# Kernel tuning notes

Measured on AMD Instinct MI355X. Metric: run time of the kernel, lower is better.

Reference implementation:

```python
import jax, jax.numpy as jnp
import numpy as np

B, S, D, H = 4, 2048, 1024, 16
HD = D // H


def setup_inputs() -> dict:
    key = jax.random.key(0)
    ks = jax.random.split(key, 12)
    sc = 1.0 / np.sqrt(D)
    inp = {
        'q': jax.random.normal(ks[0], (B, S, D), jnp.float32),
        'k': jax.random.normal(ks[1], (B, S, D), jnp.float32),
        'v': jax.random.normal(ks[2], (B, S, D), jnp.float32),
        # causal mask: 1 where masked (upper triangle), broadcasts over batch/heads
        'mask': jnp.triu(jnp.ones((S, S), jnp.float32), k=1),
        'Wq': jax.random.normal(ks[3], (D, D), jnp.float32) * sc,
        'bq': jax.random.normal(ks[4], (D,), jnp.float32) * sc,
        'Wk': jax.random.normal(ks[5], (D, D), jnp.float32) * sc,
        'bk': jax.random.normal(ks[6], (D,), jnp.float32) * sc,
        'Wv': jax.random.normal(ks[7], (D, D), jnp.float32) * sc,
        'bv': jax.random.normal(ks[8], (D,), jnp.float32) * sc,
        'Wo': jax.random.normal(ks[9], (D, D), jnp.float32) * sc,
        'bo': jax.random.normal(ks[10], (D,), jnp.float32) * sc,
    }
    return inp


def _split_heads(x):
    # [B,S,D] -> [B,H,S,HD]
    return x.reshape(B, S, H, HD).transpose(0, 2, 1, 3)


def reference(q, k, v, mask, Wq, bq, Wk, bk, Wv, bv, Wo, bo):
    qw = q @ Wq + bq
    kw = k @ Wk + bk
    vw = v @ Wv + bv
    qh, kh, vh = _split_heads(qw), _split_heads(kw), _split_heads(vw)
    scores = jnp.einsum('bhqd,bhkd->bhqk', qh, kh) / jnp.sqrt(jnp.float32(HD))
    scores = scores + mask * (-1e20)
    weights = jax.nn.softmax(scores, axis=-1)
    attn = jnp.einsum('bhqk,bhkd->bhqd', weights, vh)
    attn = attn.transpose(0, 2, 1, 3).reshape(B, S, D)
    return attn @ Wo + bo
```

## Files before the change

### kernel.cpp

```cpp
#include <hip/hip_runtime.h>
#include <hip/hip_bf16.h>
#include <stdint.h>

#define B_ 4
#define S_ 2048
#define D_ 1024
#define H_ 16
#define HD_ 64

typedef __bf16 bf16_t;
typedef __bf16 bf16x8 __attribute__((ext_vector_type(8)));
typedef __bf16 bf16x2_t __attribute__((ext_vector_type(2)));
typedef float f32x4 __attribute__((ext_vector_type(4)));
typedef int i32x4 __attribute__((ext_vector_type(4)));

#define MFMA(a, b, c) __builtin_amdgcn_mfma_f32_16x16x32_bf16((a), (b), (c), 0, 0, 0)
#define LOG2E 1.44269504088896340736f

__device__ __forceinline__ void gload_lds16(const void* g, void* l) {
  __builtin_amdgcn_global_load_lds(
      (const __attribute__((address_space(1))) uint32_t*)g,
      (__attribute__((address_space(3))) uint32_t*)l, 16, 0, 0);
}

__device__ __forceinline__ float max3f(float a, float b, float c) {
  float d;
  asm("v_max3_f32 %0, %1, %2, %3" : "=v"(d) : "v"(a), "v"(b), "v"(c));
  return d;
}

__global__ __launch_bounds__(256) void wt_kernel(const float* __restrict__ Wq,
                                                 const float* __restrict__ Wk,
                                                 const float* __restrict__ Wv,
                                                 const float* __restrict__ Wo,
                                                 bf16_t* __restrict__ wt0) {
  __shared__ float t[32][33];
  const int z = blockIdx.z;
  const float* w_ = z == 0 ? Wq : (z == 1 ? Wk : (z == 2 ? Wv : Wo));
  bf16_t* wt = wt0 + (size_t)z * (1u << 20);
  const int tx = threadIdx.x & 31, ty = threadIdx.x >> 5;
  const int n0 = blockIdx.x * 32, k0 = blockIdx.y * 32;
#pragma unroll
  for (int i = 0; i < 4; i++)
    t[ty + i * 8][tx] = w_[(size_t)(k0 + ty + i * 8) * D_ + n0 + tx];
  __syncthreads();
#pragma unroll
  for (int i = 0; i < 4; i++)
    wt[(size_t)(n0 + ty + i * 8) * D_ + k0 + tx] = (bf16_t)t[tx][ty + i * 8];
}

__global__ __launch_bounds__(256) void qkv_gemm(const float* __restrict__ qi,
                                                const float* __restrict__ ki,
                                                const float* __restrict__ vi,
                                                const bf16_t* __restrict__ wt0,
                                                const float* __restrict__ bq,
                                                const float* __restrict__ bk,
                                                const float* __restrict__ bv,
                                                bf16_t* __restrict__ out0) {
  constexpr int K = D_;
  __shared__ bf16_t smem[17408];
  bf16_t* alds = smem;
  bf16_t* blds = smem + 8192;

  const int z = blockIdx.z;
  const float* A = z == 0 ? qi : (z == 1 ? ki : vi);
  const bf16_t* WT = wt0 + (size_t)z * (1u << 20);
  const float* bias = z == 0 ? bq : (z == 1 ? bk : bv);
  bf16_t* out = out0 + (size_t)z * (8u << 20);

  const int tid = threadIdx.x;
  const int w = tid >> 6, l = tid & 63;
  const int lr = l & 15, lg = l >> 4;
  const int wm = w >> 1, wn = w & 1;
  const int ib = (int)blockIdx.y * (int)gridDim.x + (int)blockIdx.x;
  const int swz = (ib & 7) * 64 + (ib >> 3);
  const int m0 = (swz >> 3) * 128, n0 = (swz & 7) * 128;

  f32x4 acc[4][4];
#pragma unroll
  for (int mt = 0; mt < 4; mt++)
#pragma unroll
    for (int nt = 0; nt < 4; nt++) {
      f32x4 zz = {0.f, 0.f, 0.f, 0.f};
      acc[mt][nt] = zz;
    }

  for (int k0 = 0; k0 < K; k0 += 64) {
#pragma unroll
    for (int c = 0; c < 4; c++) {
      int ci = c * 256 + w * 64 + l;
      int row = ci >> 3, kc = ci & 7;
      int ks = kc ^ (row & 7);
      gload_lds16(WT + (size_t)(n0 + row) * K + k0 + ks * 8,
                  blds + (size_t)(c * 256 + w * 64) * 8);
    }
#pragma unroll
    for (int c = 0; c < 4; c++) {
      int ci = c * 256 + tid;
      int row = ci >> 3, kc = ci & 7;
      int ks = kc ^ (row & 7);
      const float* src = A + (size_t)(m0 + row) * K + k0 + ks * 8;
      float4 x0 = ((const float4*)src)[0];
      float4 x1 = ((const float4*)src)[1];
      bf16x8 vv;
      vv[0] = (bf16_t)x0.x; vv[1] = (bf16_t)x0.y; vv[2] = (bf16_t)x0.z; vv[3] = (bf16_t)x0.w;
      vv[4] = (bf16_t)x1.x; vv[5] = (bf16_t)x1.y; vv[6] = (bf16_t)x1.z; vv[7] = (bf16_t)x1.w;
      *reinterpret_cast<bf16x8*>(alds + (size_t)ci * 8) = vv;
    }
    __syncthreads();
#pragma unroll
    for (int kk = 0; kk < 2; kk++) {
      bf16x8 af[4], bfr[4];
#pragma unroll
      for (int mt = 0; mt < 4; mt++) {
        int row = wm * 64 + mt * 16 + lr;
        int kc = kk * 4 + lg;
        af[mt] = *reinterpret_cast<const bf16x8*>(alds + row * 64 + ((kc ^ (row & 7)) * 8));
      }
#pragma unroll
      for (int nt = 0; nt < 4; nt++) {
        int row = wn * 64 + nt * 16 + lr;
        int kc = kk * 4 + lg;
        bfr[nt] = *reinterpret_cast<const bf16x8*>(blds + row * 64 + ((kc ^ (row & 7)) * 8));
      }
#pragma unroll
      for (int mt = 0; mt < 4; mt++)
#pragma unroll
        for (int nt = 0; nt < 4; nt++)
          acc[mt][nt] = MFMA(af[mt], bfr[nt], acc[mt][nt]);
    }
    __syncthreads();
  }

  float bn[4];
#pragma unroll
  for (int nt = 0; nt < 4; nt++) bn[nt] = bias[n0 + wn * 64 + nt * 16 + lr];

  if (z != 2) {
    const float sc = z == 0 ? 0.125f : 1.0f;
#pragma unroll
    for (int mt = 0; mt < 4; mt++)
#pragma unroll
      for (int nt = 0; nt < 4; nt++)
#pragma unroll
        for (int r = 0; r < 4; r++) {
          int m = m0 + wm * 64 + mt * 16 + lg * 4 + r;
          int n = n0 + wn * 64 + nt * 16 + lr;
          float v = (acc[mt][nt][r] + bn[nt]) * sc;
          int b = m >> 11, s = m & 2047, h = n >> 6, hd = n & 63;
          out[(((size_t)(b * H_ + h) * S_ + s) << 6) + hd] = (bf16_t)v;
        }
  } else {
    __syncthreads();
#pragma unroll
    for (int mt = 0; mt < 4; mt++)
#pragma unroll
      for (int nt = 0; nt < 4; nt++)
#pragma unroll
        for (int r = 0; r < 4; r++) {
          int ml = wm * 64 + mt * 16 + lg * 4 + r;
          int nl = wn * 64 + nt * 16 + lr;
          smem[nl * 136 + ml] = (bf16_t)(acc[mt][nt][r] + bn[nt]);
        }
    __syncthreads();
    const int b = m0 >> 11, sbase = m0 & 2047;
#pragma unroll
    for (int c = 0; c < 8; c++) {
      int ci = c * 256 + tid;
      int dl = ci >> 4, sc2 = ci & 15;
      int n = n0 + dl, h = n >> 6, hd = n & 63;
      bf16x8 v = *reinterpret_cast<const bf16x8*>(smem + dl * 136 + sc2 * 8);
      *reinterpret_cast<bf16x8*>(out + ((size_t)((b * H_ + h) << 6) + hd) * S_ + sbase + sc2 * 8) = v;
    }
  }
}

__global__ __launch_bounds__(256) void out_gemm(const bf16_t* __restrict__ A,
                                                const bf16_t* __restrict__ WT,
                                                const float* __restrict__ bias,
                                                float* __restrict__ out) {
  constexpr int K = D_;
  __shared__ bf16_t smem[16384];
  bf16_t* alds = smem;
  bf16_t* blds = smem + 8192;

  const int tid = threadIdx.x;
  const int w = tid >> 6, l = tid & 63;
  const int lr = l & 15, lg = l >> 4;
  const int wm = w >> 1, wn = w & 1;
  const int ib = (int)blockIdx.y * (int)gridDim.x + (int)blockIdx.x;
  const int swz = (ib & 7) * 64 + (ib >> 3);
  const int m0 = (swz >> 3) * 128, n0 = (swz & 7) * 128;

  f32x4 acc[4][4];
#pragma unroll
  for (int mt = 0; mt < 4; mt++)
#pragma unroll
    for (int nt = 0; nt < 4; nt++) {
      f32x4 z = {0.f, 0.f, 0.f, 0.f};
      acc[mt][nt] = z;
    }

  for (int k0 = 0; k0 < K; k0 += 64) {
#pragma unroll
    for (int c = 0; c < 4; c++) {
      int ci = c * 256 + w * 64 + l;
      int row = ci >> 3, kc = ci & 7;
      int ks = kc ^ (row & 7);
      gload_lds16(WT + (size_t)(n0 + row) * K + k0 + ks * 8,
                  blds + (size_t)(c * 256 + w * 64) * 8);
      gload_lds16(A + (size_t)(m0 + row) * K + k0 + ks * 8,
                  alds + (size_t)(c * 256 + w * 64) * 8);
    }
    __syncthreads();
#pragma unroll
    for (int kk = 0; kk < 2; kk++) {
      bf16x8 af[4], bfr[4];
#pragma unroll
      for (int mt = 0; mt < 4; mt++) {
        int row = wm * 64 + mt * 16 + lr;
        int kc = kk * 4 + lg;
        af[mt] = *reinterpret_cast<const bf16x8*>(alds + row * 64 + ((kc ^ (row & 7)) * 8));
      }
#pragma unroll
      for (int nt = 0; nt < 4; nt++) {
        int row = wn * 64 + nt * 16 + lr;
        int kc = kk * 4 + lg;
        bfr[nt] = *reinterpret_cast<const bf16x8*>(blds + row * 64 + ((kc ^ (row & 7)) * 8));
      }
#pragma unroll
      for (int mt = 0; mt < 4; mt++)
#pragma unroll
        for (int nt = 0; nt < 4; nt++)
          acc[mt][nt] = MFMA(af[mt], bfr[nt], acc[mt][nt]);
    }
    __syncthreads();
  }

  float bn[4];
#pragma unroll
  for (int nt = 0; nt < 4; nt++) bn[nt] = bias[n0 + wn * 64 + nt * 16 + lr];
#pragma unroll
  for (int mt = 0; mt < 4; mt++)
#pragma unroll
    for (int nt = 0; nt < 4; nt++)
#pragma unroll
      for (int r = 0; r < 4; r++) {
        int m = m0 + wm * 64 + mt * 16 + lg * 4 + r;
        int n = n0 + wn * 64 + nt * 16 + lr;
        out[(size_t)m * D_ + n] = acc[mt][nt][r] + bn[nt];
      }
}

__global__ __launch_bounds__(256) void attn_k(const bf16_t* __restrict__ qh,
                                              const bf16_t* __restrict__ kh,
                                              const bf16_t* __restrict__ vt,
                                              bf16_t* __restrict__ attn) {
  __shared__ bf16_t kbuf[3][4096];
  __shared__ bf16_t vbuf[3][4096];

  const int tid = threadIdx.x, w = tid >> 6, l = tid & 63;
  const int lr = l & 15, lg = l >> 4;

  const int ib = (int)blockIdx.y * 16 + (int)blockIdx.x;
  const int xcd = ib & 7, slot = ib >> 3;
  const int bh = xcd * 8 + (slot & 7);
  const int pr = slot >> 3;
  const int b = bh >> 4, h = bh & 15;

  const int zr0 = tid >> 3, kc = tid & 7;
  const int sks = kc ^ (zr0 & 7);
  const int kprow0 = ((zr0 >> 5) & 1) * 32 + ((zr0 >> 2) & 3) * 8 + ((zr0 >> 4) & 1) * 4 + (zr0 & 3);
  const int zr1 = 32 + zr0;
  const int kprow1 = ((zr1 >> 5) & 1) * 32 + ((zr1 >> 2) & 3) * 8 + ((zr1 >> 4) & 1) * 4 + (zr1 & 3);
  const bf16_t* kbase0 = kh + ((size_t)bh * S_ + kprow0) * HD_ + sks * 8;
  const bf16_t* kbase1 = kh + ((size_t)bh * S_ + kprow1) * HD_ + sks * 8;
  const bf16_t* vbase0 = vt + ((size_t)bh * HD_ + zr0) * S_ + sks * 8;
  const bf16_t* vbase1 = vt + ((size_t)bh * HD_ + zr1) * S_ + sks * 8;

  const int xs7 = lr & 7;
  const int koffA = lr * 64 + ((lg ^ xs7) << 3);
  const int koffB = lr * 64 + (((lg ^ xs7) ^ 4) << 3);
  const int rowlim = w * 16 + lr;
  const int wsl = w * 512;

  bf16x8 ones;
#pragma unroll
  for (int i = 0; i < 8; i++) ones[i] = (bf16_t)1.0f;

  for (int half = 0; half < 2; half++) {
    const int qt = half ? (31 - pr) : pr;
    const int q0 = qt * 64 + w * 16;

    const bf16_t* qp = qh + ((size_t)bh * S_ + q0 + lr) * HD_ + lg * 8;
    bf16x8 qf0 = *(const bf16x8*)qp;
    bf16x8 qf1 = *(const bf16x8*)(qp + 32);

    float mi = -1e30f;
    f32x4 o[4], os;
#pragma unroll
    for (int nt = 0; nt < 4; nt++) {
      f32x4 z = {0.f, 0.f, 0.f, 0.f};
      o[nt] = z;
    }
    {
      f32x4 z = {0.f, 0.f, 0.f, 0.f};
      os = z;
    }

    const bf16_t *ks0 = kbase0, *ks1 = kbase1, *vs0 = vbase0, *vs1 = vbase1;
    int jsrc = 0;

#define ISSUE_STAGE(bi)                                        \
    do {                                                       \
      gload_lds16(ks0, &kbuf[bi][wsl]);                        \
      gload_lds16(ks1, &kbuf[bi][wsl + 2048]);                 \
      gload_lds16(vs0, &vbuf[bi][wsl]);                        \
      gload_lds16(vs1, &vbuf[bi][wsl + 2048]);                 \
      if (jsrc < qt) {                                         \
        ks0 += 64 * HD_; ks1 += 64 * HD_; vs0 += 64; vs1 += 64; \
        jsrc++;                                                \
      }                                                        \
    } while (0)

    ISSUE_STAGE(0);
    ISSUE_STAGE(1);
    asm volatile("s_waitcnt vmcnt(4)" ::: "memory");
    __builtin_amdgcn_s_barrier();
    __builtin_amdgcn_sched_barrier(0);

    int cidx = 0, c2 = 2;
    for (int jt = 0; jt <= qt; jt++) {
      ISSUE_STAGE(c2);
      asm volatile("s_waitcnt vmcnt(8)" ::: "memory");
      __builtin_amdgcn_s_barrier();
      __builtin_amdgcn_sched_barrier(0);

      const bf16_t* kt = kbuf[cidx];
      const bf16_t* vb = vbuf[cidx];
      f32x4 s[4];
      __builtin_amdgcn_s_setprio(1);
#pragma unroll
      for (int nt = 0; nt < 4; nt++) {
        bf16x8 kf0 = *(const bf16x8*)(kt + koffA + nt * 1024);
        bf16x8 kf1 = *(const bf16x8*)(kt + koffB + nt * 1024);
        f32x4 a = {0.f, 0.f, 0.f, 0.f};
        a = MFMA(kf0, qf0, a);
        a = MFMA(kf1, qf1, a);
        s[nt] = a;
      }
      __builtin_amdgcn_s_setprio(0);
      if (jt == qt) {
#pragma unroll
        for (int nt = 0; nt < 4; nt++) {
          int kvb = ((nt >> 1) << 5) + ((nt & 1) << 2) + lg * 8;
#pragma unroll
          for (int r = 0; r < 4; r++)
            if (kvb + r > rowlim) s[nt][r] = -1e30f;
        }
      }
      float m0 = max3f(s[0][0], s[0][1], s[0][2]);
      float m1 = max3f(s[0][3], s[1][0], s[1][1]);
      float m2 = max3f(s[1][2], s[1][3], s[2][0]);
      float m3 = max3f(s[2][1], s[2][2], s[2][3]);
      float m4 = max3f(s[3][0], s[3][1], s[3][2]);
      float mx = fmaxf(max3f(m0, m1, m2), max3f(m3, m4, s[3][3]));
      mx = fmaxf(mx, __shfl_xor(mx, 16));
      mx = fmaxf(mx, __shfl_xor(mx, 32));
      if (!__all(mx <= mi + 8.0f)) {
        float mn = fmaxf(mi, mx);
        float al = __builtin_amdgcn_exp2f((mi - mn) * LOG2E);
        mi = mn;
#pragma unroll
        for (int r = 0; r < 4; r++) {
          float alr = __shfl(al, lg * 4 + r);
          o[0][r] *= alr; o[1][r] *= alr; o[2][r] *= alr; o[3][r] *= alr;
          os[r] *= alr;
        }
      }
      const float msc = mi * LOG2E;
#pragma unroll
      for (int nt = 0; nt < 4; nt++)
#pragma unroll
        for (int r = 0; r < 4; r++)
          s[nt][r] = __builtin_amdgcn_exp2f(s[nt][r] * LOG2E - msc);
      uint32_t pk[8];
#pragma unroll
      for (int nt = 0; nt < 4; nt++) {
        bf16x2_t plo = {(bf16_t)s[nt][0], (bf16_t)s[nt][1]};
        bf16x2_t phi = {(bf16_t)s[nt][2], (bf16_t)s[nt][3]};
        pk[nt * 2] = __builtin_bit_cast(uint32_t, plo);
        pk[nt * 2 + 1] = __builtin_bit_cast(uint32_t, phi);
      }
      i32x4 w0 = {(int)pk[0], (int)pk[1], (int)pk[2], (int)pk[3]};
      i32x4 w1 = {(int)pk[4], (int)pk[5], (int)pk[6], (int)pk[7]};
      bf16x8 pa0 = __builtin_bit_cast(bf16x8, w0);
      bf16x8 pa1 = __builtin_bit_cast(bf16x8, w1);
      __builtin_amdgcn_s_setprio(1);
#pragma unroll
      for (int ntd = 0; ntd < 4; ntd++) {
        bf16x8 vf0 = *(const bf16x8*)(vb + koffA + ntd * 1024);
        bf16x8 vf1 = *(const bf16x8*)(vb + koffB + ntd * 1024);
        o[ntd] = MFMA(pa0, vf0, o[ntd]);
        o[ntd] = MFMA(pa1, vf1, o[ntd]);
      }
      os = MFMA(pa0, ones, os);
      os = MFMA(pa1, ones, os);
      __builtin_amdgcn_s_setprio(0);

      __builtin_amdgcn_sched_barrier(0);
      __builtin_amdgcn_s_barrier();
      __builtin_amdgcn_sched_barrier(0);
      cidx = (cidx == 2) ? 0 : cidx + 1;
      c2 = (c2 == 2) ? 0 : c2 + 1;
    }
#undef ISSUE_STAGE
#pragma unroll
    for (int r = 0; r < 4; r++) {
      float rinv = 1.f / os[r];
      int srw = q0 + lg * 4 + r;
#pragma unroll
      for (int ntd = 0; ntd < 4; ntd++)
        attn[((size_t)(b * S_ + srw)) * D_ + h * 64 + ntd * 16 + lr] =
            (bf16_t)(o[ntd][r] * rinv);
    }
  }
}

extern "C" void kernel_launch(void* const* d_in, const int* in_sizes, int n_in,
                              void* d_out, int out_size, void* d_ws, size_t ws_size,
                              hipStream_t stream) {
  (void)in_sizes; (void)n_in; (void)out_size; (void)ws_size;
  const float* q  = (const float*)d_in[0];
  const float* k  = (const float*)d_in[1];
  const float* v  = (const float*)d_in[2];
  const float* Wq = (const float*)d_in[4];
  const float* bq = (const float*)d_in[5];
  const float* Wk = (const float*)d_in[6];
  const float* bk = (const float*)d_in[7];
  const float* Wv = (const float*)d_in[8];
  const float* bv = (const float*)d_in[9];
  const float* Wo = (const float*)d_in[10];
  const float* bo = (const float*)d_in[11];

  char* ws = (char*)d_ws;
  bf16_t* wt0 = (bf16_t*)(ws + (0ull << 20));
  bf16_t* wto = (bf16_t*)(ws + (6ull << 20));
  bf16_t* qhb = (bf16_t*)(ws + (8ull << 20));
  bf16_t* khb = (bf16_t*)(ws + (24ull << 20));
  bf16_t* vtb = (bf16_t*)(ws + (40ull << 20));
  bf16_t* atb = (bf16_t*)(ws + (56ull << 20));

  dim3 tb(256);
  wt_kernel<<<dim3(32, 32, 4), tb, 0, stream>>>(Wq, Wk, Wv, Wo, wt0);
  qkv_gemm<<<dim3(8, 64, 3), tb, 0, stream>>>(q, k, v, wt0, bq, bk, bv, qhb);
  attn_k<<<dim3(16, 64), tb, 0, stream>>>(qhb, khb, vtb, atb);
  out_gemm<<<dim3(8, 64), tb, 0, stream>>>(atb, wto, bo, (float*)d_out);
}
```

Baseline: 193.4 us.

## Pre-convert QKV inputs to bf16 and double-buffer GEMM loads via direct-to-LDS

Adds a separate elementwise kernel that converts the fp32 q/k/v inputs to bf16 up front. Both projection GEMMs can then use a single templated kernel that loads A and B straight into LDS with global_load_lds. The GEMM main loop becomes a two-stage double-buffered pipeline using explicit vmcnt waits and barriers, so the next tile's loads overlap the MFMA work. The cost is an extra launch plus a write and re-read of a 48 MB bf16 copy of the inputs, and the workspace layout is rearranged so the attention output reuses the conversion buffer.

Result: faster. 186.7 us (-3.5%).

```diff
diff --git a/kernel.cpp b/kernel.cpp
--- a/kernel.cpp
+++ b/kernel.cpp
@@ -49,32 +49,49 @@
     wt[(size_t)(n0 + ty + i * 8) * D_ + k0 + tx] = (bf16_t)t[tx][ty + i * 8];
 }
 
-__global__ __launch_bounds__(256) void qkv_gemm(const float* __restrict__ qi,
-                                                const float* __restrict__ ki,
-                                                const float* __restrict__ vi,
-                                                const bf16_t* __restrict__ wt0,
-                                                const float* __restrict__ bq,
-                                                const float* __restrict__ bk,
-                                                const float* __restrict__ bv,
-                                                bf16_t* __restrict__ out0) {
-  constexpr int K = D_;
-  __shared__ bf16_t smem[17408];
-  bf16_t* alds = smem;
-  bf16_t* blds = smem + 8192;
-
+__global__ __launch_bounds__(256) void conv_kernel(const float* __restrict__ q,
+                                                   const float* __restrict__ k,
+                                                   const float* __restrict__ v,
+                                                   bf16_t* __restrict__ out) {
   const int z = blockIdx.z;
-  const float* A = z == 0 ? qi : (z == 1 ? ki : vi);
-  const bf16_t* WT = wt0 + (size_t)z * (1u << 20);
-  const float* bias = z == 0 ? bq : (z == 1 ? bk : bv);
-  bf16_t* out = out0 + (size_t)z * (8u << 20);
+  const float* src = z == 0 ? q : (z == 1 ? k : v);
+  bf16_t* dst = out + (size_t)z * 8388608u;
+  const size_t i = ((size_t)blockIdx.x * 256 + threadIdx.x) * 8;
+  float4 x0 = *(const float4*)(src + i);
+  float4 x1 = *(const float4*)(src + i + 4);
+  bf16x8 vv;
+  vv[0] = (bf16_t)x0.x; vv[1] = (bf16_t)x0.y; vv[2] = (bf16_t)x0.z; vv[3] = (bf16_t)x0.w;
+  vv[4] = (bf16_t)x1.x; vv[5] = (bf16_t)x1.y; vv[6] = (bf16_t)x1.z; vv[7] = (bf16_t)x1.w;
+  *(bf16x8*)(dst + i) = vv;
+}
+
+template <bool QKV>
+__global__ __launch_bounds__(256) void mm_kernel(const bf16_t* __restrict__ A0,
+                                                 const bf16_t* __restrict__ wt0,
+                                                 const float* __restrict__ b0,
+                                                 const float* __restrict__ b1,
+                                                 const float* __restrict__ b2,
+                                                 void* __restrict__ out0) {
+  __shared__ bf16_t smem[32768];
+
+  const int z = QKV ? blockIdx.z : 0;
+  const bf16_t* A = A0 + (size_t)z * 8388608u;
+  const bf16_t* WT = wt0 + (size_t)z * 1048576u;
+  const float* bias = QKV ? (z == 0 ? b0 : (z == 1 ? b1 : b2)) : b0;
 
   const int tid = threadIdx.x;
   const int w = tid >> 6, l = tid & 63;
   const int lr = l & 15, lg = l >> 4;
   const int wm = w >> 1, wn = w & 1;
-  const int ib = (int)blockIdx.y * (int)gridDim.x + (int)blockIdx.x;
+  const int ib = (int)blockIdx.y * 8 + (int)blockIdx.x;
   const int swz = (ib & 7) * 64 + (ib >> 3);
   const int m0 = (swz >> 3) * 128, n0 = (swz & 7) * 128;
+
+  const int row0 = tid >> 3;
+  const int ks = (tid & 7) ^ (row0 & 7);
+  const bf16_t* aS = A + (size_t)(m0 + row0) * 1024 + ks * 8;
+  const bf16_t* bS = WT + (size_t)(n0 + row0) * 1024 + ks * 8;
+  const int wsl = w * 512;
 
   f32x4 acc[4][4];
 #pragma unroll
@@ -85,29 +102,26 @@
       acc[mt][nt] = zz;
     }
 
-  for (int k0 = 0; k0 < K; k0 += 64) {
-#pragma unroll
-    for (int c = 0; c < 4; c++) {
-      int ci = c * 256 + w * 64 + l;
-      int row = ci >> 3, kc = ci & 7;
-      int ks = kc ^ (row & 7);
-      gload_lds16(WT + (size_t)(n0 + row) * K + k0 + ks * 8,
-                  blds + (size_t)(c * 256 + w * 64) * 8);
-    }
-#pragma unroll
-    for (int c = 0; c < 4; c++) {
-      int ci = c * 256 + tid;
-      int row = ci >> 3, kc = ci & 7;
-      int ks = kc ^ (row & 7);
-      const float* src = A + (size_t)(m0 + row) * K + k0 + ks * 8;
-      float4 x0 = ((const float4*)src)[0];
-      float4 x1 = ((const float4*)src)[1];
-      bf16x8 vv;
-      vv[0] = (bf16_t)x0.x; vv[1] = (bf16_t)x0.y; vv[2] = (bf16_t)x0.z; vv[3] = (bf16_t)x0.w;
-      vv[4] = (bf16_t)x1.x; vv[5] = (bf16_t)x1.y; vv[6] = (bf16_t)x1.z; vv[7] = (bf16_t)x1.w;
-      *reinterpret_cast<bf16x8*>(alds + (size_t)ci * 8) = vv;
-    }
-    __syncthreads();
+#define STAGE(bi, kt)                                                   \
+  do {                                                                  \
+    bf16_t* ad = smem + (bi) * 16384 + wsl;                             \
+    bf16_t* bd = smem + (bi) * 16384 + 8192 + wsl;                      \
+    _Pragma("unroll") for (int c = 0; c < 4; c++) {                     \
+      gload_lds16(bS + (size_t)c * 32768 + (kt), bd + c * 2048);        \
+      gload_lds16(aS + (size_t)c * 32768 + (kt), ad + c * 2048);        \
+    }                                                                   \
+  } while (0)
+
+  STAGE(0, 0);
+  STAGE(1, 64);
+  asm volatile("s_waitcnt vmcnt(8)" ::: "memory");
+  __builtin_amdgcn_s_barrier();
+  __builtin_amdgcn_sched_barrier(0);
+
+  int buf = 0;
+  for (int jt = 0; jt < 16; ++jt) {
+    const bf16_t* alds = smem + buf * 16384;
+    const bf16_t* blds = alds + 8192;
 #pragma unroll
     for (int kk = 0; kk < 2; kk++) {
       bf16x8 af[4], bfr[4];
@@ -129,14 +143,37 @@
         for (int nt = 0; nt < 4; nt++)
           acc[mt][nt] = MFMA(af[mt], bfr[nt], acc[mt][nt]);
     }
-    __syncthreads();
+    if (jt == 15) break;
+    __builtin_amdgcn_sched_barrier(0);
+    __builtin_amdgcn_s_barrier();
+    __builtin_amdgcn_sched_barrier(0);
+    const int tn = (jt + 2 < 16) ? jt + 2 : 15;
+    STAGE(buf, tn * 64);
+    asm volatile("s_waitcnt vmcnt(8)" ::: "memory");
+    __builtin_amdgcn_s_barrier();
+    __builtin_amdgcn_sched_barrier(0);
+    buf ^= 1;
   }
+#undef STAGE
 
   float bn[4];
 #pragma unroll
   for (int nt = 0; nt < 4; nt++) bn[nt] = bias[n0 + wn * 64 + nt * 16 + lr];
 
-  if (z != 2) {
+  if (!QKV) {
+    float* out = (float*)out0;
+#pragma unroll
+    for (int mt = 0; mt < 4; mt++)
+#pragma unroll
+      for (int nt = 0; nt < 4; nt++)
+#pragma unroll
+        for (int r = 0; r < 4; r++) {
+          int m = m0 + wm * 64 + mt * 16 + lg * 4 + r;
+          int n = n0 + wn * 64 + nt * 16 + lr;
+          out[(size_t)m * D_ + n] = acc[mt][nt][r] + bn[nt];
+        }
+  } else if (z != 2) {
+    bf16_t* out = (bf16_t*)out0 + (size_t)z * 8388608u;
     const float sc = z == 0 ? 0.125f : 1.0f;
 #pragma unroll
     for (int mt = 0; mt < 4; mt++)
@@ -151,6 +188,7 @@
           out[(((size_t)(b * H_ + h) * S_ + s) << 6) + hd] = (bf16_t)v;
         }
   } else {
+    bf16_t* out = (bf16_t*)out0 + (size_t)z * 8388608u;
     __syncthreads();
 #pragma unroll
     for (int mt = 0; mt < 4; mt++)
@@ -173,83 +211,6 @@
       *reinterpret_cast<bf16x8*>(out + ((size_t)((b * H_ + h) << 6) + hd) * S_ + sbase + sc2 * 8) = v;
     }
   }
-}
-
-__global__ __launch_bounds__(256) void out_gemm(const bf16_t* __restrict__ A,
-                                                const bf16_t* __restrict__ WT,
-                                                const float* __restrict__ bias,
-                                                float* __restrict__ out) {
-  constexpr int K = D_;
-  __shared__ bf16_t smem[16384];
-  bf16_t* alds = smem;
-  bf16_t* blds = smem + 8192;
-
-  const int tid = threadIdx.x;
-  const int w = tid >> 6, l = tid & 63;
-  const int lr = l & 15, lg = l >> 4;
-  const int wm = w >> 1, wn = w & 1;
-  const int ib = (int)blockIdx.y * (int)gridDim.x + (int)blockIdx.x;
-  const int swz = (ib & 7) * 64 + (ib >> 3);
-  const int m0 = (swz >> 3) * 128, n0 = (swz & 7) * 128;
-
-  f32x4 acc[4][4];
-#pragma unroll
-  for (int mt = 0; mt < 4; mt++)
-#pragma unroll
-    for (int nt = 0; nt < 4; nt++) {
-      f32x4 z = {0.f, 0.f, 0.f, 0.f};
-      acc[mt][nt] = z;
-    }
-
-  for (int k0 = 0; k0 < K; k0 += 64) {
-#pragma unroll
-    for (int c = 0; c < 4; c++) {
-      int ci = c * 256 + w * 64 + l;
-      int row = ci >> 3, kc = ci & 7;
-      int ks = kc ^ (row & 7);
-      gload_lds16(WT + (size_t)(n0 + row) * K + k0 + ks * 8,
-                  blds + (size_t)(c * 256 + w * 64) * 8);
-      gload_lds16(A + (size_t)(m0 + row) * K + k0 + ks * 8,
-                  alds + (size_t)(c * 256 + w * 64) * 8);
-    }
-    __syncthreads();
-#pragma unroll
-    for (int kk = 0; kk < 2; kk++) {
-      bf16x8 af[4], bfr[4];
-#pragma unroll
-      for (int mt = 0; mt < 4; mt++) {
-        int row = wm * 64 + mt * 16 + lr;
-        int kc = kk * 4 + lg;
-        af[mt] = *reinterpret_cast<const bf16x8*>(alds + row * 64 + ((kc ^ (row & 7)) * 8));
-      }
-#pragma unroll
-      for (int nt = 0; nt < 4; nt++) {
-        int row = wn * 64 + nt * 16 + lr;
-        int kc = kk * 4 + lg;
-        bfr[nt] = *reinterpret_cast<const bf16x8*>(blds + row * 64 + ((kc ^ (row & 7)) * 8));
-      }
-#pragma unroll
-      for (int mt = 0; mt < 4; mt++)
-#pragma unroll
-        for (int nt = 0; nt < 4; nt++)
-          acc[mt][nt] = MFMA(af[mt], bfr[nt], acc[mt][nt]);
-    }
-    __syncthreads();
-  }
-
-  float bn[4];
-#pragma unroll
-  for (int nt = 0; nt < 4; nt++) bn[nt] = bias[n0 + wn * 64 + nt * 16 + lr];
-#pragma unroll
-  for (int mt = 0; mt < 4; mt++)
-#pragma unroll
-    for (int nt = 0; nt < 4; nt++)
-#pragma unroll
-      for (int r = 0; r < 4; r++) {
-        int m = m0 + wm * 64 + mt * 16 + lg * 4 + r;
-        int n = n0 + wn * 64 + nt * 16 + lr;
-        out[(size_t)m * D_ + n] = acc[mt][nt][r] + bn[nt];
-      }
 }
 
 __global__ __launch_bounds__(256) void attn_k(const bf16_t* __restrict__ qh,
@@ -444,16 +405,18 @@
   const float* bo = (const float*)d_in[11];
 
   char* ws = (char*)d_ws;
-  bf16_t* wt0 = (bf16_t*)(ws + (0ull << 20));
-  bf16_t* wto = (bf16_t*)(ws + (6ull << 20));
-  bf16_t* qhb = (bf16_t*)(ws + (8ull << 20));
-  bf16_t* khb = (bf16_t*)(ws + (24ull << 20));
-  bf16_t* vtb = (bf16_t*)(ws + (40ull << 20));
-  bf16_t* atb = (bf16_t*)(ws + (56ull << 20));
+  bf16_t* wt0  = (bf16_t*)(ws + (0ull << 20));
+  bf16_t* wto  = (bf16_t*)(ws + (6ull << 20));
+  bf16_t* qkvb = (bf16_t*)(ws + (8ull << 20));
+  bf16_t* qhb  = (bf16_t*)(ws + (56ull << 20));
+  bf16_t* khb  = (bf16_t*)(ws + (72ull << 20));
+  bf16_t* vtb  = (bf16_t*)(ws + (88ull << 20));
+  bf16_t* atb  = (bf16_t*)(ws + (8ull << 20));
 
   dim3 tb(256);
   wt_kernel<<<dim3(32, 32, 4), tb, 0, stream>>>(Wq, Wk, Wv, Wo, wt0);
-  qkv_gemm<<<dim3(8, 64, 3), tb, 0, stream>>>(q, k, v, wt0, bq, bk, bv, qhb);
+  conv_kernel<<<dim3(4096, 1, 3), tb, 0, stream>>>(q, k, v, qkvb);
+  mm_kernel<true><<<dim3(8, 64, 3), tb, 0, stream>>>(qkvb, wt0, bq, bk, bv, qhb);
   attn_k<<<dim3(16, 64), tb, 0, stream>>>(qhb, khb, vtb, atb);
-  out_gemm<<<dim3(8, 64), tb, 0, stream>>>(atb, wto, bo, (float*)d_out);
-}
+  mm_kernel<false><<<dim3(8, 64), tb, 0, stream>>>(atb, wto, bo, nullptr, nullptr, d_out);
+}
```
